# Kernel tuning notes

Hardware: AMD Instinct MI355X
Metric: run time of the kernel (lower is better)

The kernel has to match this reference:

```python
import jax, jax.numpy as jnp
import numpy as np

B, S, D, H = 4, 2048, 1024, 16
HD = D // H

def setup_inputs() -> dict:
    key = jax.random.key(0)
    ks = jax.random.split(key, 9)
    s = 1.0 / np.sqrt(D)
    return {
        "x": jax.random.normal(ks[0], (B, S, D), dtype=jnp.float32),
        "wq": jax.random.uniform(ks[1], (D, D), jnp.float32, -s, s),
        "bq": jnp.zeros((D,), jnp.float32),
        "wk": jax.random.uniform(ks[2], (D, D), jnp.float32, -s, s),
        "bk": jnp.zeros((D,), jnp.float32),
        "wv": jax.random.uniform(ks[3], (D, D), jnp.float32, -s, s),
        "bv": jnp.zeros((D,), jnp.float32),
        "wo": jax.random.uniform(ks[4], (D, D), jnp.float32, -s, s),
        "bo": jnp.zeros((D,), jnp.float32),
    }

def reference(x, wq, bq, wk, bk, wv, bv, wo, bo):
    b, s, _ = x.shape
    # project and split heads: [B,S,D] -> [B,H,S,HD]
    def heads(w, bias):
        return (x @ w.T + bias).reshape(b, s, H, HD).transpose(0, 2, 1, 3)
    q = heads(wq, bq)
    k = heads(wk, bk)
    v = heads(wv, bv)
    scale = 1.0 / jnp.sqrt(jnp.float32(HD))
    scores = jnp.einsum("bhqd,bhkd->bhqk", q, k) * scale
    attn = jax.nn.softmax(scores, axis=-1)
    out = jnp.einsum("bhqk,bhkd->bhqd", attn, v)
    out = out.transpose(0, 2, 1, 3).reshape(b, s, D)
    return out @ wo.T + bo
```

## Files before the change

### kernel.cpp

```cpp
#include <hip/hip_runtime.h>
#include <stdint.h>


#define B_ 4
#define S_ 2048
#define D_ 1024
#define H_ 16
#define HD_ 64
#define M_ (B_ * S_)

typedef __bf16 bf16x8 __attribute__((ext_vector_type(8)));
typedef float f32x4 __attribute__((ext_vector_type(4)));
typedef float f32x16 __attribute__((ext_vector_type(16)));
typedef unsigned short u16;

#define QSCALE 0.18033688011112042f
#define THR2 11.0f

__device__ __forceinline__ u16 f2bf(float f) {
  union { float f; unsigned u; } v; v.f = f;
  unsigned u = v.u;
  u += 0x7fff + ((u >> 16) & 1);
  return (u16)(u >> 16);
}

__device__ __forceinline__ float exp2_fast(float x) {
#if __has_builtin(__builtin_amdgcn_exp2f)
  return __builtin_amdgcn_exp2f(x);
#else
  return __expf(x * 0.69314718056f);
#endif
}

__device__ __forceinline__ unsigned packbf(float a, float b) {
  union { unsigned u; __bf16 h[2]; } v;
  v.h[0] = (__bf16)a; v.h[1] = (__bf16)b;
  return v.u;
}

__device__ __forceinline__ void gl2lds16(const void* g, void* l) {
  __builtin_amdgcn_global_load_lds(
      (const __attribute__((address_space(1))) unsigned int*)g,
      (__attribute__((address_space(3))) unsigned int*)l, 16, 0, 0);
}

__global__ __launch_bounds__(256) void convert_kernel(
    const float* __restrict__ x, const float* __restrict__ wq,
    const float* __restrict__ wk, const float* __restrict__ wv,
    const float* __restrict__ wo, u16* __restrict__ xb, u16* __restrict__ wqb,
    u16* __restrict__ wkb, u16* __restrict__ wvb, u16* __restrict__ wob) {
  const int64_t NX = (int64_t)M_ * D_ / 4;
  const int64_t NW = (int64_t)D_ * D_ / 4;
  int64_t i = (int64_t)blockIdx.x * blockDim.x + threadIdx.x;
  const float* src; u16* dst; int64_t off;
  if (i < NX)              { src = x;  dst = xb;  off = i; }
  else if (i < NX + NW)    { src = wq; dst = wqb; off = i - NX; }
  else if (i < NX + 2*NW)  { src = wk; dst = wkb; off = i - NX - NW; }
  else if (i < NX + 3*NW)  { src = wv; dst = wvb; off = i - NX - 2*NW; }
  else                     { src = wo; dst = wob; off = i - NX - 3*NW; }
  float4 v = reinterpret_cast<const float4*>(src)[off];
  ushort4 o;
  o.x = f2bf(v.x); o.y = f2bf(v.y); o.z = f2bf(v.z); o.w = f2bf(v.w);
  reinterpret_cast<ushort4*>(dst)[off] = o;
}

template <int MODE>
__global__ __launch_bounds__(256) void gemm_kernel(
    const u16* __restrict__ A, const u16* __restrict__ Bw,
    const float* __restrict__ bias, void* __restrict__ out) {
  __shared__ u16 As[128 * 64];
  __shared__ u16 Bs[128 * 64];
  const int tid = threadIdx.x;
  const int lane = tid & 63;
  const int wid = tid >> 6;
  const int row0 = blockIdx.y * 128;
  const int col0 = blockIdx.x * 128;
  const int wr = (wid >> 1) * 64;
  const int wc = (wid & 1) * 64;

  f32x4 acc[4][4] = {};
  const int srow = lane >> 3;
  const int cc = (lane & 7) ^ srow;

  for (int kt = 0; kt < D_; kt += 64) {
    __syncthreads();
    for (int t = 0; t < 4; ++t) {
      int r = (wid * 4 + t) * 8 + srow;
      gl2lds16(A + (int64_t)(row0 + r) * D_ + kt + cc * 8,
               (char*)As + (wid * 4 + t) * 1024);
      gl2lds16(Bw + (int64_t)(col0 + r) * D_ + kt + cc * 8,
               (char*)Bs + (wid * 4 + t) * 1024);
    }
    __syncthreads();

    bf16x8 af[4][2], bfr[4][2];
#pragma unroll
    for (int mi = 0; mi < 4; ++mi)
#pragma unroll
      for (int ks = 0; ks < 2; ++ks) {
        int c = ks * 4 + (lane >> 4);
        int ra = wr + mi * 16 + (lane & 15);
        af[mi][ks] = *reinterpret_cast<const bf16x8*>(
            (char*)As + ra * 128 + ((c ^ (ra & 7)) << 4));
        int rb = wc + mi * 16 + (lane & 15);
        bfr[mi][ks] = *reinterpret_cast<const bf16x8*>(
            (char*)Bs + rb * 128 + ((c ^ (rb & 7)) << 4));
      }
#pragma unroll
    for (int ks = 0; ks < 2; ++ks)
#pragma unroll
      for (int mi = 0; mi < 4; ++mi)
#pragma unroll
        for (int ni = 0; ni < 4; ++ni) {
          if (MODE == 1)
            acc[mi][ni] = __builtin_amdgcn_mfma_f32_16x16x32_bf16(
                bfr[ni][ks], af[mi][ks], acc[mi][ni], 0, 0, 0);
          else
            acc[mi][ni] = __builtin_amdgcn_mfma_f32_16x16x32_bf16(
                af[mi][ks], bfr[ni][ks], acc[mi][ni], 0, 0, 0);
        }
  }

  if (MODE == 0 || MODE == 3) {
    u16* o = (u16*)out;
#pragma unroll
    for (int mi = 0; mi < 4; ++mi)
#pragma unroll
      for (int ni = 0; ni < 4; ++ni) {
        int j = col0 + wc + ni * 16 + (lane & 15);
        float bvv = bias[j];
        int h = j >> 6, hd = j & 63;
#pragma unroll
        for (int r = 0; r < 4; ++r) {
          int i = row0 + wr + mi * 16 + (lane >> 4) * 4 + r;
          int b = i >> 11, s = i & 2047;
          float val = acc[mi][ni][r] + bvv;
          if (MODE == 3) val *= QSCALE;
          o[((int64_t)(b * H_ + h) * S_ + s) * HD_ + hd] = f2bf(val);
        }
      }
  } else if (MODE == 1) {
    u16* o = (u16*)out;
#pragma unroll
    for (int mi = 0; mi < 4; ++mi)
#pragma unroll
      for (int ni = 0; ni < 4; ++ni) {
        int i = row0 + wr + mi * 16 + (lane & 15);
        int b = i >> 11, s = i & 2047;
#pragma unroll
        for (int r = 0; r < 4; ++r) {
          int j = col0 + wc + ni * 16 + (lane >> 4) * 4 + r;
          int h = j >> 6, hd = j & 63;
          o[((int64_t)(b * H_ + h) * HD_ + hd) * S_ + s] = f2bf(acc[mi][ni][r] + bias[j]);
        }
      }
  } else {
    float* o = (float*)out;
#pragma unroll
    for (int mi = 0; mi < 4; ++mi)
#pragma unroll
      for (int ni = 0; ni < 4; ++ni) {
        int j = col0 + wc + ni * 16 + (lane & 15);
        float bvv = bias[j];
#pragma unroll
        for (int r = 0; r < 4; ++r) {
          int i = row0 + wr + mi * 16 + (lane >> 4) * 4 + r;
          o[(int64_t)i * D_ + j] = acc[mi][ni][r] + bvv;
        }
      }
  }
}

__global__ __launch_bounds__(512) void attn_kernel(
    const u16* __restrict__ Q, const u16* __restrict__ Kg,
    const u16* __restrict__ Vt, u16* __restrict__ AO) {
  __shared__ u16 Ks[2][64 * 64];
  __shared__ u16 Vs[2][64 * 64];
  const int tid = threadIdx.x;
  const int lane = tid & 63;
  const int l31 = lane & 31;
  const int hi = lane >> 5;
  const int wid = tid >> 6;
  const int orig = blockIdx.x;
  const int swz = (orig & 7) * 64 + (orig >> 3);
  const int bh = swz >> 3;
  const int qw = (swz & 7) * 256 + wid * 32;

  bf16x8 qf[4];
#pragma unroll
  for (int ks = 0; ks < 4; ++ks)
    qf[ks] = *reinterpret_cast<const bf16x8*>(
        Q + ((int64_t)bh * S_ + qw + l31) * HD_ + ks * 16 + hi * 8);

  bf16x8 ones8;
#pragma unroll
  for (int i = 0; i < 8; ++i) ones8[i] = (__bf16)1.0f;

  f32x16 o0 = {}, o1 = {}, ls = {};
  float mrow = -1e30f;

  const int srow = lane >> 3;
  const int cc = (lane & 7) ^ srow;

  const u16* kp = Kg + ((int64_t)bh * S_ + wid * 8 + srow) * HD_ + cc * 8;
  const u16* vp = Vt + ((int64_t)bh * HD_ + wid * 8 + srow) * S_ + cc * 8;

  gl2lds16(kp, (char*)Ks[0] + wid * 1024); kp += 64 * HD_;
  gl2lds16(vp, (char*)Vs[0] + wid * 1024); vp += 64;

  const int NT = S_ / 64;

#define TILE_STEP(T, CUR)                                                      \
  {                                                                            \
    asm volatile("s_waitcnt vmcnt(0)" ::: "memory");                           \
    __builtin_amdgcn_s_barrier();                                              \
    if ((T) + 1 < NT) {                                                        \
      gl2lds16(kp, (char*)Ks[(CUR) ^ 1] + wid * 1024);                         \
      gl2lds16(vp, (char*)Vs[(CUR) ^ 1] + wid * 1024);                         \
      kp += 64 * HD_; vp += 64;                                                \
    }                                                                          \
    f32x16 sc0 = {}, sc1 = {};                                                 \
    {                                                                          \
      const char* kbase = (const char*)Ks[CUR];                                \
      __builtin_amdgcn_s_setprio(1);                                           \
      _Pragma("unroll")                                                        \
      for (int ks = 0; ks < 4; ++ks) {                                         \
        int chunk = 2 * ks + hi;                                               \
        int r0 = l31, r1 = 32 + l31;                                           \
        bf16x8 k0 = *reinterpret_cast<const bf16x8*>(                          \
            kbase + r0 * 128 + ((chunk ^ (r0 & 7)) << 4));                     \
        bf16x8 k1 = *reinterpret_cast<const bf16x8*>(                          \
            kbase + r1 * 128 + ((chunk ^ (r1 & 7)) << 4));                     \
        sc0 = __builtin_amdgcn_mfma_f32_32x32x16_bf16(k0, qf[ks], sc0, 0, 0, 0); \
        sc1 = __builtin_amdgcn_mfma_f32_32x32x16_bf16(k1, qf[ks], sc1, 0, 0, 0); \
      }                                                                        \
      __builtin_amdgcn_s_setprio(0);                                           \
    }                                                                          \
    float a8[8];                                                               \
    _Pragma("unroll")                                                          \
    for (int i = 0; i < 8; ++i)                                                \
      a8[i] = fmaxf(fmaxf(fmaxf(sc0[2 * i], sc0[2 * i + 1]), sc1[2 * i]),      \
                    sc1[2 * i + 1]);                                           \
    float mx = fmaxf(fmaxf(fmaxf(fmaxf(a8[0], a8[1]), a8[2]), a8[3]),          \
                     fmaxf(fmaxf(fmaxf(a8[4], a8[5]), a8[6]), a8[7]));         \
    if (!__all((mx - mrow <= THR2) ? 1 : 0)) {                                 \
      float mxf = fmaxf(mx, __shfl_xor(mx, 32));                               \
      float mnew = fmaxf(mrow, mxf);                                           \
      float al = exp2_fast(mrow - mnew);                                       \
      mrow = mnew;                                                             \
      _Pragma("unroll")                                                        \
      for (int tt = 0; tt < 16; ++tt) {                                        \
        float at = __shfl(al, (tt & 3) + 8 * (tt >> 2) + 4 * hi);              \
        o0[tt] *= at; o1[tt] *= at; ls[tt] *= at;                              \
      }                                                                        \
    }                                                                          \
    _Pragma("unroll")                                                          \
    for (int tt = 0; tt < 16; ++tt) {                                          \
      sc0[tt] = exp2_fast(sc0[tt] - mrow);                                     \
      sc1[tt] = exp2_fast(sc1[tt] - mrow);                                     \
    }                                                                          \
    unsigned w0[4][2], w1[4][2];                                               \
    _Pragma("unroll")                                                          \
    for (int rr = 0; rr < 4; ++rr) {                                           \
      w0[rr][0] = packbf(sc0[4 * rr], sc0[4 * rr + 1]);                        \
      w0[rr][1] = packbf(sc0[4 * rr + 2], sc0[4 * rr + 3]);                    \
      w1[rr][0] = packbf(sc1[4 * rr], sc1[4 * rr + 1]);                        \
      w1[rr][1] = packbf(sc1[4 * rr + 2], sc1[4 * rr + 3]);                    \
    }                                                                          \
    unsigned rv0[2][2], rv1[2][2];                                             \
    _Pragma("unroll")                                                          \
    for (int c = 0; c < 2; ++c) {                                              \
      _Pragma("unroll")                                                        \
      for (int h2 = 0; h2 < 2; ++h2) {                                         \
        rv0[c][h2] = (unsigned)__shfl_xor(                                     \
            (int)(hi ? w0[2 * c][h2] : w0[2 * c + 1][h2]), 32);                \
        rv1[c][h2] = (unsigned)__shfl_xor(                                     \
            (int)(hi ? w1[2 * c][h2] : w1[2 * c + 1][h2]), 32);                \
      }                                                                        \
    }                                                                          \
    {                                                                          \
      const char* vbase = (const char*)Vs[CUR];                                \
      __builtin_amdgcn_s_setprio(1);                                           \
      _Pragma("unroll")                                                        \
      for (int kb = 0; kb < 4; ++kb) {                                         \
        const int c = kb & 1;                                                  \
        union { bf16x8 v; unsigned u[4]; } pu;                                 \
        if (kb < 2) {                                                          \
          pu.u[0] = hi ? rv0[c][0] : w0[2 * c][0];                             \
          pu.u[1] = hi ? rv0[c][1] : w0[2 * c][1];                             \
          pu.u[2] = hi ? w0[2 * c + 1][0] : rv0[c][0];                         \
          pu.u[3] = hi ? w0[2 * c + 1][1] : rv0[c][1];                         \
        } else {                                                               \
          pu.u[0] = hi ? rv1[c][0] : w1[2 * c][0];                             \
          pu.u[1] = hi ? rv1[c][1] : w1[2 * c][1];                             \
          pu.u[2] = hi ? w1[2 * c + 1][0] : rv1[c][0];                         \
          pu.u[3] = hi ? w1[2 * c + 1][1] : rv1[c][1];                         \
        }                                                                      \
        int chunk = 2 * kb + hi;                                               \
        int r0 = l31, r1 = 32 + l31;                                           \
        bf16x8 v0 = *reinterpret_cast<const bf16x8*>(                          \
            vbase + r0 * 128 + ((chunk ^ (r0 & 7)) << 4));                     \
        bf16x8 v1 = *reinterpret_cast<const bf16x8*>(                          \
            vbase + r1 * 128 + ((chunk ^ (r1 & 7)) << 4));                     \
        o0 = __builtin_amdgcn_mfma_f32_32x32x16_bf16(pu.v, v0, o0, 0, 0, 0);   \
        o1 = __builtin_amdgcn_mfma_f32_32x32x16_bf16(pu.v, v1, o1, 0, 0, 0);   \
        ls = __builtin_amdgcn_mfma_f32_32x32x16_bf16(pu.v, ones8, ls, 0, 0, 0);\
      }                                                                        \
      __builtin_amdgcn_s_setprio(0);                                           \
    }                                                                          \
  }

  for (int t = 0; t < NT; t += 2) {
    TILE_STEP(t, 0)
    TILE_STEP(t + 1, 1)
  }
#undef TILE_STEP

  const int b = bh >> 4, h = bh & 15;
#pragma unroll
  for (int tt = 0; tt < 16; ++tt) {
    int row = (tt & 3) + 8 * (tt >> 2) + 4 * hi;
    float inv = __builtin_amdgcn_rcpf(ls[tt]);
    int qr = qw + row;
    int64_t base = ((int64_t)(b * S_ + qr)) * D_ + h * HD_ + l31;
    AO[base] = f2bf(o0[tt] * inv);
    AO[base + 32] = f2bf(o1[tt] * inv);
  }
}

extern "C" void kernel_launch(void* const* d_in, const int* in_sizes, int n_in,
                              void* d_out, int out_size, void* d_ws, size_t ws_size,
                              hipStream_t stream) {
  const float* x  = (const float*)d_in[0];
  const float* wq = (const float*)d_in[1];
  const float* bq = (const float*)d_in[2];
  const float* wk = (const float*)d_in[3];
  const float* bk = (const float*)d_in[4];
  const float* wv = (const float*)d_in[5];
  const float* bv = (const float*)d_in[6];
  const float* wo = (const float*)d_in[7];
  const float* bo = (const float*)d_in[8];
  char* ws = (char*)d_ws;
  u16* xb  = (u16*)ws;
  u16* wqb = (u16*)(ws + (16ll << 20));
  u16* wkb = (u16*)(ws + (18ll << 20));
  u16* wvb = (u16*)(ws + (20ll << 20));
  u16* wob = (u16*)(ws + (22ll << 20));
  u16* q   = (u16*)(ws + (24ll << 20));
  u16* k   = (u16*)(ws + (40ll << 20));
  u16* vt  = (u16*)(ws + (56ll << 20));
  u16* ao  = xb;

  convert_kernel<<<12288, 256, 0, stream>>>(x, wq, wk, wv, wo, xb, wqb, wkb, wvb, wob);
  dim3 gg(D_ / 128, M_ / 128);
  gemm_kernel<3><<<gg, 256, 0, stream>>>(xb, wqb, bq, q);
  gemm_kernel<0><<<gg, 256, 0, stream>>>(xb, wkb, bk, k);
  gemm_kernel<1><<<gg, 256, 0, stream>>>(xb, wvb, bv, vt);
  attn_kernel<<<512, 512, 0, stream>>>(q, k, vt, ao);
  gemm_kernel<2><<<gg, 256, 0, stream>>>(ao, wob, bo, (float*)d_out);
}
```

Measured before the change: 245.3 us.

## Process two 32-row query blocks per wave in attention to reuse K/V tiles

After: 224.3 us. 1.09x faster.

```diff
diff --git a/kernel.cpp b/kernel.cpp
--- a/kernel.cpp
+++ b/kernel.cpp
@@ -171,7 +171,7 @@
   }
 }
 
-__global__ __launch_bounds__(512) void attn_kernel(
+__global__ __launch_bounds__(512, 2) void attn_kernel(
     const u16* __restrict__ Q, const u16* __restrict__ Kg,
     const u16* __restrict__ Vt, u16* __restrict__ AO) {
   __shared__ u16 Ks[2][64 * 64];
@@ -182,22 +182,24 @@
   const int hi = lane >> 5;
   const int wid = tid >> 6;
   const int orig = blockIdx.x;
-  const int swz = (orig & 7) * 64 + (orig >> 3);
-  const int bh = swz >> 3;
-  const int qw = (swz & 7) * 256 + wid * 32;
-
-  bf16x8 qf[4];
-#pragma unroll
-  for (int ks = 0; ks < 4; ++ks)
-    qf[ks] = *reinterpret_cast<const bf16x8*>(
-        Q + ((int64_t)bh * S_ + qw + l31) * HD_ + ks * 16 + hi * 8);
+  const int swz = (orig & 7) * 32 + (orig >> 3);
+  const int bh = swz >> 2;
+  const int qw = (swz & 3) * 512 + wid * 64;
+
+  bf16x8 qf[2][4];
+#pragma unroll
+  for (int qb = 0; qb < 2; ++qb)
+#pragma unroll
+    for (int ks = 0; ks < 4; ++ks)
+      qf[qb][ks] = *reinterpret_cast<const bf16x8*>(
+          Q + ((int64_t)bh * S_ + qw + qb * 32 + l31) * HD_ + ks * 16 + hi * 8);
 
   bf16x8 ones8;
 #pragma unroll
   for (int i = 0; i < 8; ++i) ones8[i] = (__bf16)1.0f;
 
-  f32x16 o0 = {}, o1 = {}, ls = {};
-  float mrow = -1e30f;
+  f32x16 o0[2] = {}, o1[2] = {}, ls[2] = {};
+  float mrow[2] = {-1e30f, -1e30f};
 
   const int srow = lane >> 3;
   const int cc = (lane & 7) ^ srow;
@@ -219,7 +221,7 @@
       gl2lds16(vp, (char*)Vs[(CUR) ^ 1] + wid * 1024);                         \
       kp += 64 * HD_; vp += 64;                                                \
     }                                                                          \
-    f32x16 sc0 = {}, sc1 = {};                                                 \
+    f32x16 sc0[2] = {{}, {}}, sc1[2] = {{}, {}};                               \
     {                                                                          \
       const char* kbase = (const char*)Ks[CUR];                                \
       __builtin_amdgcn_s_setprio(1);                                           \
@@ -231,51 +233,67 @@
             kbase + r0 * 128 + ((chunk ^ (r0 & 7)) << 4));                     \
         bf16x8 k1 = *reinterpret_cast<const bf16x8*>(                          \
             kbase + r1 * 128 + ((chunk ^ (r1 & 7)) << 4));                     \
-        sc0 = __builtin_amdgcn_mfma_f32_32x32x16_bf16(k0, qf[ks], sc0, 0, 0, 0); \
-        sc1 = __builtin_amdgcn_mfma_f32_32x32x16_bf16(k1, qf[ks], sc1, 0, 0, 0); \
+        _Pragma("unroll")                                                      \
+        for (int qb = 0; qb < 2; ++qb) {                                       \
+          sc0[qb] = __builtin_amdgcn_mfma_f32_32x32x16_bf16(k0, qf[qb][ks],    \
+                                                            sc0[qb], 0, 0, 0); \
+          sc1[qb] = __builtin_amdgcn_mfma_f32_32x32x16_bf16(k1, qf[qb][ks],    \
+                                                            sc1[qb], 0, 0, 0); \
+        }                                                                      \
       }                                                                        \
       __builtin_amdgcn_s_setprio(0);                                           \
     }                                                                          \
-    float a8[8];                                                               \
+    float mx[2];                                                               \
     _Pragma("unroll")                                                          \
-    for (int i = 0; i < 8; ++i)                                                \
-      a8[i] = fmaxf(fmaxf(fmaxf(sc0[2 * i], sc0[2 * i + 1]), sc1[2 * i]),      \
-                    sc1[2 * i + 1]);                                           \
-    float mx = fmaxf(fmaxf(fmaxf(fmaxf(a8[0], a8[1]), a8[2]), a8[3]),          \
+    for (int qb = 0; qb < 2; ++qb) {                                           \
+      float a8[8];                                                             \
+      _Pragma("unroll")                                                        \
+      for (int i = 0; i < 8; ++i)                                              \
+        a8[i] = fmaxf(fmaxf(fmaxf(sc0[qb][2 * i], sc0[qb][2 * i + 1]),         \
+                            sc1[qb][2 * i]), sc1[qb][2 * i + 1]);              \
+      mx[qb] = fmaxf(fmaxf(fmaxf(fmaxf(a8[0], a8[1]), a8[2]), a8[3]),          \
                      fmaxf(fmaxf(fmaxf(a8[4], a8[5]), a8[6]), a8[7]));         \
-    if (!__all((mx - mrow <= THR2) ? 1 : 0)) {                                 \
-      float mxf = fmaxf(mx, __shfl_xor(mx, 32));                               \
-      float mnew = fmaxf(mrow, mxf);                                           \
-      float al = exp2_fast(mrow - mnew);                                       \
-      mrow = mnew;                                                             \
+    }                                                                          \
+    int okd = (mx[0] - mrow[0] <= THR2 && mx[1] - mrow[1] <= THR2) ? 1 : 0;    \
+    if (!__all(okd)) {                                                         \
+      _Pragma("unroll")                                                        \
+      for (int qb = 0; qb < 2; ++qb) {                                         \
+        float mxf = fmaxf(mx[qb], __shfl_xor(mx[qb], 32));                     \
+        float mnew = fmaxf(mrow[qb], mxf);                                     \
+        float al = exp2_fast(mrow[qb] - mnew);                                 \
+        mrow[qb] = mnew;                                                       \
+        _Pragma("unroll")                                                      \
+        for (int tt = 0; tt < 16; ++tt) {                                      \
+          float at = __shfl(al, (tt & 3) + 8 * (tt >> 2) + 4 * hi);            \
+          o0[qb][tt] *= at; o1[qb][tt] *= at; ls[qb][tt] *= at;                \
+        }                                                                      \
+      }                                                                        \
+    }                                                                          \
+    unsigned w[2][2][4][2], rv[2][2][2][2];                                    \
+    _Pragma("unroll")                                                          \
+    for (int qb = 0; qb < 2; ++qb) {                                           \
       _Pragma("unroll")                                                        \
       for (int tt = 0; tt < 16; ++tt) {                                        \
-        float at = __shfl(al, (tt & 3) + 8 * (tt >> 2) + 4 * hi);              \
-        o0[tt] *= at; o1[tt] *= at; ls[tt] *= at;                              \
-      }                                                                        \
-    }                                                                          \
-    _Pragma("unroll")                                                          \
-    for (int tt = 0; tt < 16; ++tt) {                                          \
-      sc0[tt] = exp2_fast(sc0[tt] - mrow);                                     \
-      sc1[tt] = exp2_fast(sc1[tt] - mrow);                                     \
-    }                                                                          \
-    unsigned w0[4][2], w1[4][2];                                               \
-    _Pragma("unroll")                                                          \
-    for (int rr = 0; rr < 4; ++rr) {                                           \
-      w0[rr][0] = packbf(sc0[4 * rr], sc0[4 * rr + 1]);                        \
-      w0[rr][1] = packbf(sc0[4 * rr + 2], sc0[4 * rr + 3]);                    \
-      w1[rr][0] = packbf(sc1[4 * rr], sc1[4 * rr + 1]);                        \
-      w1[rr][1] = packbf(sc1[4 * rr + 2], sc1[4 * rr + 3]);                    \
-    }                                                                          \
-    unsigned rv0[2][2], rv1[2][2];                                             \
-    _Pragma("unroll")                                                          \
-    for (int c = 0; c < 2; ++c) {                                              \
-      _Pragma("unroll")                                                        \
-      for (int h2 = 0; h2 < 2; ++h2) {                                         \
-        rv0[c][h2] = (unsigned)__shfl_xor(                                     \
-            (int)(hi ? w0[2 * c][h2] : w0[2 * c + 1][h2]), 32);                \
-        rv1[c][h2] = (unsigned)__shfl_xor(                                     \
-            (int)(hi ? w1[2 * c][h2] : w1[2 * c + 1][h2]), 32);                \
+        sc0[qb][tt] = exp2_fast(sc0[qb][tt] - mrow[qb]);                       \
+        sc1[qb][tt] = exp2_fast(sc1[qb][tt] - mrow[qb]);                       \
+      }                                                                        \
+      _Pragma("unroll")                                                        \
+      for (int rr = 0; rr < 4; ++rr) {                                         \
+        w[qb][0][rr][0] = packbf(sc0[qb][4 * rr], sc0[qb][4 * rr + 1]);        \
+        w[qb][0][rr][1] = packbf(sc0[qb][4 * rr + 2], sc0[qb][4 * rr + 3]);    \
+        w[qb][1][rr][0] = packbf(sc1[qb][4 * rr], sc1[qb][4 * rr + 1]);        \
+        w[qb][1][rr][1] = packbf(sc1[qb][4 * rr + 2], sc1[qb][4 * rr + 3]);    \
+      }                                                                        \
+      _Pragma("unroll")                                                        \
+      for (int n2 = 0; n2 < 2; ++n2) {                                         \
+        _Pragma("unroll")                                                      \
+        for (int c = 0; c < 2; ++c) {                                          \
+          _Pragma("unroll")                                                    \
+          for (int h2 = 0; h2 < 2; ++h2)                                       \
+            rv[qb][n2][c][h2] = (unsigned)__shfl_xor(                          \
+                (int)(hi ? w[qb][n2][2 * c][h2] : w[qb][n2][2 * c + 1][h2]),   \
+                32);                                                           \
+        }                                                                      \
       }                                                                        \
     }                                                                          \
     {                                                                          \
@@ -283,28 +301,27 @@
       __builtin_amdgcn_s_setprio(1);                                           \
       _Pragma("unroll")                                                        \
       for (int kb = 0; kb < 4; ++kb) {                                         \
-        const int c = kb & 1;                                                  \
-        union { bf16x8 v; unsigned u[4]; } pu;                                 \
-        if (kb < 2) {                                                          \
-          pu.u[0] = hi ? rv0[c][0] : w0[2 * c][0];                             \
-          pu.u[1] = hi ? rv0[c][1] : w0[2 * c][1];                             \
-          pu.u[2] = hi ? w0[2 * c + 1][0] : rv0[c][0];                         \
-          pu.u[3] = hi ? w0[2 * c + 1][1] : rv0[c][1];                         \
-        } else {                                                               \
-          pu.u[0] = hi ? rv1[c][0] : w1[2 * c][0];                             \
-          pu.u[1] = hi ? rv1[c][1] : w1[2 * c][1];                             \
-          pu.u[2] = hi ? w1[2 * c + 1][0] : rv1[c][0];                         \
-          pu.u[3] = hi ? w1[2 * c + 1][1] : rv1[c][1];                         \
-        }                                                                      \
+        const int c = kb & 1, n2 = kb >> 1;                                    \
         int chunk = 2 * kb + hi;                                               \
         int r0 = l31, r1 = 32 + l31;                                           \
         bf16x8 v0 = *reinterpret_cast<const bf16x8*>(                          \
             vbase + r0 * 128 + ((chunk ^ (r0 & 7)) << 4));                     \
         bf16x8 v1 = *reinterpret_cast<const bf16x8*>(                          \
             vbase + r1 * 128 + ((chunk ^ (r1 & 7)) << 4));                     \
-        o0 = __builtin_amdgcn_mfma_f32_32x32x16_bf16(pu.v, v0, o0, 0, 0, 0);   \
-        o1 = __builtin_amdgcn_mfma_f32_32x32x16_bf16(pu.v, v1, o1, 0, 0, 0);   \
-        ls = __builtin_amdgcn_mfma_f32_32x32x16_bf16(pu.v, ones8, ls, 0, 0, 0);\
+        _Pragma("unroll")                                                      \
+        for (int qb = 0; qb < 2; ++qb) {                                       \
+          union { bf16x8 v; unsigned u[4]; } pu;                               \
+          pu.u[0] = hi ? rv[qb][n2][c][0] : w[qb][n2][2 * c][0];               \
+          pu.u[1] = hi ? rv[qb][n2][c][1] : w[qb][n2][2 * c][1];               \
+          pu.u[2] = hi ? w[qb][n2][2 * c + 1][0] : rv[qb][n2][c][0];           \
+          pu.u[3] = hi ? w[qb][n2][2 * c + 1][1] : rv[qb][n2][c][1];           \
+          o0[qb] = __builtin_amdgcn_mfma_f32_32x32x16_bf16(pu.v, v0, o0[qb],   \
+                                                           0, 0, 0);           \
+          o1[qb] = __builtin_amdgcn_mfma_f32_32x32x16_bf16(pu.v, v1, o1[qb],   \
+                                                           0, 0, 0);           \
+          ls[qb] = __builtin_amdgcn_mfma_f32_32x32x16_bf16(pu.v, ones8,        \
+                                                           ls[qb], 0, 0, 0);   \
+        }                                                                      \
       }                                                                        \
       __builtin_amdgcn_s_setprio(0);                                           \
     }                                                                          \
@@ -318,14 +335,16 @@
 
   const int b = bh >> 4, h = bh & 15;
 #pragma unroll
-  for (int tt = 0; tt < 16; ++tt) {
-    int row = (tt & 3) + 8 * (tt >> 2) + 4 * hi;
-    float inv = __builtin_amdgcn_rcpf(ls[tt]);
-    int qr = qw + row;
-    int64_t base = ((int64_t)(b * S_ + qr)) * D_ + h * HD_ + l31;
-    AO[base] = f2bf(o0[tt] * inv);
-    AO[base + 32] = f2bf(o1[tt] * inv);
-  }
+  for (int qb = 0; qb < 2; ++qb)
+#pragma unroll
+    for (int tt = 0; tt < 16; ++tt) {
+      int row = (tt & 3) + 8 * (tt >> 2) + 4 * hi;
+      float inv = __builtin_amdgcn_rcpf(ls[qb][tt]);
+      int qr = qw + qb * 32 + row;
+      int64_t base = ((int64_t)(b * S_ + qr)) * D_ + h * HD_ + l31;
+      AO[base] = f2bf(o0[qb][tt] * inv);
+      AO[base + 32] = f2bf(o1[qb][tt] * inv);
+    }
 }
 
 extern "C" void kernel_launch(void* const* d_in, const int* in_sizes, int n_in,
@@ -356,6 +375,6 @@
   gemm_kernel<3><<<gg, 256, 0, stream>>>(xb, wqb, bq, q);
   gemm_kernel<0><<<gg, 256, 0, stream>>>(xb, wkb, bk, k);
   gemm_kernel<1><<<gg, 256, 0, stream>>>(xb, wvb, bv, vt);
-  attn_kernel<<<512, 512, 0, stream>>>(q, k, vt, ao);
+  attn_kernel<<<256, 512, 0, stream>>>(q, k, vt, ao);
   gemm_kernel<2><<<gg, 256, 0, stream>>>(ao, wob, bo, (float*)d_out);
 }
```
